# Optimization experiments

Measured on AMD Instinct MI355X. Metric: run time of the kernel, lower is better.

## Reference

```python
import jax, jax.numpy as jnp
import numpy as np

H = 1024

def setup_inputs() -> dict:
    key = jax.random.key(0)
    ks = jax.random.split(key, 7)
    B, S = 64, 2048
    decoder_hidden = jax.random.normal(ks[0], (B, H), dtype=jnp.float32)
    encoder_outputs = jax.random.normal(ks[1], (B, S, H), dtype=jnp.float32)
    sc = 1.0 / np.sqrt(H)
    W1_w = jax.random.normal(ks[2], (H, H), dtype=jnp.float32) * sc
    W1_b = jax.random.normal(ks[3], (H,), dtype=jnp.float32) * sc
    W2_w = jax.random.normal(ks[4], (H, H), dtype=jnp.float32) * sc
    W2_b = jax.random.normal(ks[5], (H,), dtype=jnp.float32) * sc
    v_w = jax.random.normal(ks[6], (H,), dtype=jnp.float32) * sc
    return {"decoder_hidden": decoder_hidden, "encoder_outputs": encoder_outputs,
            "W1_w": W1_w, "W1_b": W1_b, "W2_w": W2_w, "W2_b": W2_b, "v_w": v_w}

def reference(decoder_hidden, encoder_outputs, W1_w, W1_b, W2_w, W2_b, v_w):
    # enc proj: [B,S,H] @ [H,H] ; dec proj: [B,H] @ [H,H], broadcast over S
    enc_proj = jnp.einsum('bsh,hk->bsk', encoder_outputs, W1_w) + W1_b
    dec_proj = decoder_hidden @ W2_w + W2_b  # [B,H]
    e = jnp.tanh(enc_proj + dec_proj[:, None, :])  # [B,S,H]
    scores = jnp.einsum('bsh,h->bs', e, v_w)  # [B,S]
    attn_weights = jax.nn.softmax(scores, axis=1)
    context = jnp.einsum('bs,bsh->bh', attn_weights, encoder_outputs)
    return (context, attn_weights)
```

## Files before the change

### kernel.cpp

```cpp
#include <hip/hip_runtime.h>
#include <hip/hip_bf16.h>
#include <hip/hip_fp16.h>

#define HDIM 1024
#define BATCH 64
#define SEQ 2048
#define MTOT (BATCH*SEQ)
#define BM 128
#define BN 128
#define BK 32

typedef float f32x4 __attribute__((ext_vector_type(4)));
typedef _Float16 half8 __attribute__((ext_vector_type(8)));

static __device__ __forceinline__ void gload_lds16(const void* g, void* l) {
  __builtin_amdgcn_global_load_lds((const __attribute__((address_space(1))) void*)g,
                                   (__attribute__((address_space(3))) void*)l, 16, 0, 0);
}

__global__ void k_w1t(const float* __restrict__ W1, unsigned short* __restrict__ W1T) {
  __shared__ float tile[64][65];
  int h0 = blockIdx.x * 64, k0 = blockIdx.y * 64;
  int t = threadIdx.x;
#pragma unroll
  for (int j = 0; j < 4; ++j) {
    int q = j * 256 + t, r = q >> 4, c = (q & 15) * 4;
    float4 v = *(const float4*)(W1 + (size_t)(h0 + r) * HDIM + k0 + c);
    tile[r][c + 0] = v.x; tile[r][c + 1] = v.y; tile[r][c + 2] = v.z; tile[r][c + 3] = v.w;
  }
  __syncthreads();
#pragma unroll
  for (int j = 0; j < 4; ++j) {
    int q = j * 256 + t, r = q >> 4, c = (q & 15) * 4;
    union { _Float16 h[4]; ushort4 u; } cv;
    cv.h[0] = (_Float16)tile[c + 0][r];
    cv.h[1] = (_Float16)tile[c + 1][r];
    cv.h[2] = (_Float16)tile[c + 2][r];
    cv.h[3] = (_Float16)tile[c + 3][r];
    *(ushort4*)(W1T + (size_t)(k0 + r) * HDIM + h0 + c) = cv.u;
  }
}

__global__ void k_decproj(const float* __restrict__ dh, const float* __restrict__ W2,
                          const float* __restrict__ W2b, float* __restrict__ dp) {
  __shared__ float drow[HDIM];
  int b = blockIdx.x, t = threadIdx.x;
#pragma unroll
  for (int j = 0; j < 4; ++j) drow[j * 256 + t] = dh[(size_t)b * HDIM + j * 256 + t];
  __syncthreads();
  f32x4 acc = {0.f, 0.f, 0.f, 0.f};
#pragma unroll 16
  for (int h = 0; h < HDIM; ++h) {
    float d = drow[h];
    f32x4 w = *(const f32x4*)(W2 + (size_t)h * HDIM + t * 4);
    acc += w * d;
  }
  acc += *(const f32x4*)(W2b + t * 4);
  *(f32x4*)(dp + (size_t)b * HDIM + t * 4) = acc;
}

__global__ __launch_bounds__(256, 2) void k_scores(
    const float* __restrict__ E, const unsigned short* __restrict__ W1T,
    const float* __restrict__ W1b, const float* __restrict__ dp,
    const float* __restrict__ vw, float* __restrict__ spart) {
  __shared__ unsigned short As[BM * BK];
  __shared__ unsigned short Bs[BN * BK];
  __shared__ float biasv[BN], vv[BN];
  __shared__ float scr[BM][2];

  int t = threadIdx.x;
  int bid = blockIdx.x;
  int xcd = bid & 7;
  int q = bid >> 3;
  int mt = (xcd << 7) + (q >> 3);
  int nt = q & 7;
  int m0 = mt * BM, n0 = nt * BN;
  int b = m0 >> 11;

  if (t < BN) {
    int k = n0 + t;
    biasv[t] = W1b[k] + dp[(size_t)b * HDIM + k];
    vv[t] = vw[k];
  }

  int lane = t & 63, wid = t >> 6;
  int wr = wid >> 1, wc = wid & 1;
  int l15 = lane & 15, l4 = lane >> 4;

  f32x4 acc[4][4];
#pragma unroll
  for (int i = 0; i < 4; ++i)
#pragma unroll
    for (int j = 0; j < 4; ++j) acc[i][j] = {0.f, 0.f, 0.f, 0.f};

  const float* Abase = E + (size_t)m0 * HDIM;

  for (int kt = 0; kt < HDIM / BK; ++kt) {
#pragma unroll
    for (int j = 0; j < 4; ++j) {
      int q2 = j * 256 + t;
      int r = q2 >> 3, c = (q2 & 7) * 4;
      float4 v = *(const float4*)(Abase + (size_t)r * HDIM + kt * BK + c);
      union { _Float16 h[4]; unsigned long long u; } cv;
      cv.h[0] = (_Float16)v.x; cv.h[1] = (_Float16)v.y;
      cv.h[2] = (_Float16)v.z; cv.h[3] = (_Float16)v.w;
      *(unsigned long long*)&As[q2 * 4] = cv.u;
    }
#pragma unroll
    for (int j = 0; j < 2; ++j) {
      const unsigned short* g = W1T + (size_t)(n0 + (wid * 2 + j) * 16) * HDIM
                              + (size_t)(lane >> 2) * HDIM
                              + kt * BK + (lane & 3) * 8;
      gload_lds16(g, (char*)Bs + (size_t)(wid * 2 + j) * 1024);
    }
    __syncthreads();

    half8 af[4], bf[4];
#pragma unroll
    for (int mi = 0; mi < 4; ++mi)
      af[mi] = *(const half8*)&As[(wr * 64 + mi * 16 + l15) * BK + l4 * 8];
#pragma unroll
    for (int ni = 0; ni < 4; ++ni)
      bf[ni] = *(const half8*)&Bs[(wc * 64 + ni * 16 + l15) * BK + l4 * 8];
#pragma unroll
    for (int mi = 0; mi < 4; ++mi)
#pragma unroll
      for (int ni = 0; ni < 4; ++ni)
        acc[mi][ni] = __builtin_amdgcn_mfma_f32_16x16x32_f16(af[mi], bf[ni], acc[mi][ni], 0, 0, 0);
    __syncthreads();
  }

  float bias_l[4], v_l[4];
#pragma unroll
  for (int ni = 0; ni < 4; ++ni) {
    bias_l[ni] = biasv[wc * 64 + ni * 16 + l15];
    v_l[ni] = vv[wc * 64 + ni * 16 + l15];
  }
#pragma unroll
  for (int mi = 0; mi < 4; ++mi) {
#pragma unroll
    for (int r = 0; r < 4; ++r) {
      float s = 0.f;
#pragma unroll
      for (int ni = 0; ni < 4; ++ni) {
        float x = acc[mi][ni][r] + bias_l[ni];
        float ex = __expf(2.f * x);
        float th = 1.f - 2.f / (ex + 1.f);
        s += th * v_l[ni];
      }
      s += __shfl_xor(s, 1); s += __shfl_xor(s, 2);
      s += __shfl_xor(s, 4); s += __shfl_xor(s, 8);
      if (l15 == 0) scr[wr * 64 + mi * 16 + l4 * 4 + r][wc] = s;
    }
  }
  __syncthreads();
  if (t < BM) spart[((size_t)m0 + t) * 8 + nt] = scr[t][0] + scr[t][1];
}

__global__ void k_softmax(const float* __restrict__ spart, float* __restrict__ attn) {
  __shared__ float sc[SEQ];
  __shared__ float red[8];
  int b = blockIdx.x, t = threadIdx.x;
  float mx = -1e30f;
#pragma unroll
  for (int j = 0; j < 8; ++j) {
    int s = j * 256 + t;
    const f32x4* p = (const f32x4*)(spart + ((size_t)b * SEQ + s) * 8);
    f32x4 x = p[0], y = p[1];
    float v = (x[0] + x[1]) + (x[2] + x[3]) + (y[0] + y[1]) + (y[2] + y[3]);
    sc[s] = v;
    mx = fmaxf(mx, v);
  }
  for (int m = 1; m < 64; m <<= 1) mx = fmaxf(mx, __shfl_xor(mx, m));
  if ((t & 63) == 0) red[t >> 6] = mx;
  __syncthreads();
  mx = fmaxf(fmaxf(red[0], red[1]), fmaxf(red[2], red[3]));
  float w[8]; float sum = 0.f;
#pragma unroll
  for (int j = 0; j < 8; ++j) {
    float e = __expf(sc[j * 256 + t] - mx);
    w[j] = e; sum += e;
  }
  for (int m = 1; m < 64; m <<= 1) sum += __shfl_xor(sum, m);
  if ((t & 63) == 0) red[4 + (t >> 6)] = sum;
  __syncthreads();
  float inv = 1.f / (red[4] + red[5] + red[6] + red[7]);
#pragma unroll
  for (int j = 0; j < 8; ++j)
    attn[(size_t)b * SEQ + j * 256 + t] = w[j] * inv;
}

__global__ void k_ctx_part(const float* __restrict__ E, const float* __restrict__ attn,
                           float* __restrict__ cpart) {
  int b = blockIdx.x >> 4, ch = blockIdx.x & 15;
  int t = threadIdx.x;
  const float* wrow = attn + (size_t)b * SEQ + ch * 128;
  const float* Eb = E + ((size_t)b * SEQ + ch * 128) * HDIM;
  f32x4 acc = {0.f, 0.f, 0.f, 0.f};
#pragma unroll 4
  for (int s = 0; s < 128; ++s) {
    float w = wrow[s];
    f32x4 e = *(const f32x4*)(Eb + (size_t)s * HDIM + t * 4);
    acc += e * w;
  }
  *(f32x4*)(cpart + (size_t)blockIdx.x * HDIM + t * 4) = acc;
}

__global__ void k_ctx_reduce(const float* __restrict__ cpart, float* __restrict__ ctx) {
  int idx = blockIdx.x * 256 + threadIdx.x;
  int b = idx >> 10, k = idx & 1023;
  float s = 0.f;
#pragma unroll
  for (int c = 0; c < 16; ++c) s += cpart[((size_t)(b * 16 + c)) * HDIM + k];
  ctx[idx] = s;
}

extern "C" void kernel_launch(void* const* d_in, const int* in_sizes, int n_in,
                              void* d_out, int out_size, void* d_ws, size_t ws_size,
                              hipStream_t stream) {
  const float* dh  = (const float*)d_in[0];
  const float* E   = (const float*)d_in[1];
  const float* W1w = (const float*)d_in[2];
  const float* W1b = (const float*)d_in[3];
  const float* W2w = (const float*)d_in[4];
  const float* W2b = (const float*)d_in[5];
  const float* vw  = (const float*)d_in[6];
  float* out  = (float*)d_out;
  float* ctx  = out;
  float* attn = out + BATCH * HDIM;

  char* ws = (char*)d_ws;
  unsigned short* W1T = (unsigned short*)ws;
  float* dp    = (float*)(ws + (2u << 20));
  float* spart = (float*)(ws + (2u << 20) + (256u << 10));
  float* cpart = (float*)(ws + (6u << 20) + (256u << 10));

  k_w1t<<<dim3(16, 16), 256, 0, stream>>>(W1w, W1T);
  k_decproj<<<BATCH, 256, 0, stream>>>(dh, W2w, W2b, dp);
  k_scores<<<(MTOT / BM) * (HDIM / BN), 256, 0, stream>>>(E, W1T, W1b, dp, vw, spart);
  k_softmax<<<BATCH, 256, 0, stream>>>(spart, attn);
  k_ctx_part<<<BATCH * 16, 256, 0, stream>>>(E, attn, cpart);
  k_ctx_reduce<<<256, 256, 0, stream>>>(cpart, ctx);
}
```

Measured before the change: 592.4 us.

## Stream fp32 activations into LDS directly with swizzle, widen K tile, split context more

The score GEMM now loads fp32 encoder tiles straight into LDS with async global-to-LDS copies, using an XOR swizzle to avoid bank conflicts. The fp16 conversion moves to the point where fragments are read from LDS, and BK grows to 64 with two MFMA k-steps per tile. The launch-bounds occupancy hint of 2 is dropped, and the B tile uses a swizzled layout too. The context reduction splits each sequence into 32 chunks when the workspace is large enough, giving more parallelism. The trade-off is doubled LDS per block (fp32 A tile, larger BK), which may lower occupancy, and conversion work repeated per wave in exchange for cutting register staging and VALU work in the load path.

```diff
diff --git a/kernel.cpp b/kernel.cpp
--- a/kernel.cpp
+++ b/kernel.cpp
@@ -8,7 +8,7 @@
 #define MTOT (BATCH*SEQ)
 #define BM 128
 #define BN 128
-#define BK 32
+#define BK 64
 
 typedef float f32x4 __attribute__((ext_vector_type(4)));
 typedef _Float16 half8 __attribute__((ext_vector_type(8)));
@@ -59,11 +59,11 @@
   *(f32x4*)(dp + (size_t)b * HDIM + t * 4) = acc;
 }
 
-__global__ __launch_bounds__(256, 2) void k_scores(
+__global__ __launch_bounds__(256) void k_scores(
     const float* __restrict__ E, const unsigned short* __restrict__ W1T,
     const float* __restrict__ W1b, const float* __restrict__ dp,
     const float* __restrict__ vw, float* __restrict__ spart) {
-  __shared__ unsigned short As[BM * BK];
+  __shared__ float As[BM * BK];
   __shared__ unsigned short Bs[BN * BK];
   __shared__ float biasv[BN], vv[BN];
   __shared__ float scr[BM][2];
@@ -93,40 +93,54 @@
 #pragma unroll
     for (int j = 0; j < 4; ++j) acc[i][j] = {0.f, 0.f, 0.f, 0.f};
 
-  const float* Abase = E + (size_t)m0 * HDIM;
-
   for (int kt = 0; kt < HDIM / BK; ++kt) {
 #pragma unroll
+    for (int j = 0; j < 8; ++j) {
+      int chunk = wid * 8 + j;
+      int row = chunk * 4 + (lane >> 4);
+      int r15 = ((chunk & 3) << 2) + (lane >> 4);
+      int u = (lane & 15) ^ r15;
+      const float* g = E + (size_t)(m0 + row) * HDIM + kt * BK + u * 4;
+      gload_lds16(g, (char*)As + (size_t)chunk * 1024);
+    }
+#pragma unroll
     for (int j = 0; j < 4; ++j) {
-      int q2 = j * 256 + t;
-      int r = q2 >> 3, c = (q2 & 7) * 4;
-      float4 v = *(const float4*)(Abase + (size_t)r * HDIM + kt * BK + c);
-      union { _Float16 h[4]; unsigned long long u; } cv;
-      cv.h[0] = (_Float16)v.x; cv.h[1] = (_Float16)v.y;
-      cv.h[2] = (_Float16)v.z; cv.h[3] = (_Float16)v.w;
-      *(unsigned long long*)&As[q2 * 4] = cv.u;
-    }
-#pragma unroll
-    for (int j = 0; j < 2; ++j) {
-      const unsigned short* g = W1T + (size_t)(n0 + (wid * 2 + j) * 16) * HDIM
-                              + (size_t)(lane >> 2) * HDIM
-                              + kt * BK + (lane & 3) * 8;
-      gload_lds16(g, (char*)Bs + (size_t)(wid * 2 + j) * 1024);
+      int chunk = wid * 4 + j;
+      int row = chunk * 8 + (lane >> 3);
+      int u = (lane & 7) ^ (lane >> 3);
+      const unsigned short* g = W1T + (size_t)(n0 + row) * HDIM + kt * BK + u * 8;
+      gload_lds16(g, (char*)Bs + (size_t)chunk * 1024);
     }
     __syncthreads();
 
-    half8 af[4], bf[4];
-#pragma unroll
-    for (int mi = 0; mi < 4; ++mi)
-      af[mi] = *(const half8*)&As[(wr * 64 + mi * 16 + l15) * BK + l4 * 8];
-#pragma unroll
-    for (int ni = 0; ni < 4; ++ni)
-      bf[ni] = *(const half8*)&Bs[(wc * 64 + ni * 16 + l15) * BK + l4 * 8];
-#pragma unroll
-    for (int mi = 0; mi < 4; ++mi)
-#pragma unroll
-      for (int ni = 0; ni < 4; ++ni)
-        acc[mi][ni] = __builtin_amdgcn_mfma_f32_16x16x32_f16(af[mi], bf[ni], acc[mi][ni], 0, 0, 0);
+#pragma unroll
+    for (int ks = 0; ks < 2; ++ks) {
+      half8 af[4], bf[4];
+#pragma unroll
+      for (int mi = 0; mi < 4; ++mi) {
+        int row = wr * 64 + mi * 16 + l15;
+        int ua = ks * 8 + l4 * 2;
+        f32x4 va = *(const f32x4*)((const char*)As + row * 256 + (((ua    ) ^ l15) << 4));
+        f32x4 vb = *(const f32x4*)((const char*)As + row * 256 + (((ua + 1) ^ l15) << 4));
+        union { _Float16 h[8]; half8 v; } cv;
+        cv.h[0] = (_Float16)va[0]; cv.h[1] = (_Float16)va[1];
+        cv.h[2] = (_Float16)va[2]; cv.h[3] = (_Float16)va[3];
+        cv.h[4] = (_Float16)vb[0]; cv.h[5] = (_Float16)vb[1];
+        cv.h[6] = (_Float16)vb[2]; cv.h[7] = (_Float16)vb[3];
+        af[mi] = cv.v;
+      }
+#pragma unroll
+      for (int ni = 0; ni < 4; ++ni) {
+        int row = wc * 64 + ni * 16 + l15;
+        int u = ks * 4 + l4;
+        bf[ni] = *(const half8*)((const char*)Bs + row * 128 + ((u ^ (l15 & 7)) << 4));
+      }
+#pragma unroll
+      for (int mi = 0; mi < 4; ++mi)
+#pragma unroll
+        for (int ni = 0; ni < 4; ++ni)
+          acc[mi][ni] = __builtin_amdgcn_mfma_f32_16x16x32_f16(af[mi], bf[ni], acc[mi][ni], 0, 0, 0);
+    }
     __syncthreads();
   }
 
@@ -191,14 +205,14 @@
 }
 
 __global__ void k_ctx_part(const float* __restrict__ E, const float* __restrict__ attn,
-                           float* __restrict__ cpart) {
-  int b = blockIdx.x >> 4, ch = blockIdx.x & 15;
+                           float* __restrict__ cpart, int nch, int rpc) {
+  int b = blockIdx.x / nch, ch = blockIdx.x % nch;
   int t = threadIdx.x;
-  const float* wrow = attn + (size_t)b * SEQ + ch * 128;
-  const float* Eb = E + ((size_t)b * SEQ + ch * 128) * HDIM;
+  const float* wrow = attn + (size_t)b * SEQ + (size_t)ch * rpc;
+  const float* Eb = E + ((size_t)b * SEQ + (size_t)ch * rpc) * HDIM;
   f32x4 acc = {0.f, 0.f, 0.f, 0.f};
 #pragma unroll 4
-  for (int s = 0; s < 128; ++s) {
+  for (int s = 0; s < rpc; ++s) {
     float w = wrow[s];
     f32x4 e = *(const f32x4*)(Eb + (size_t)s * HDIM + t * 4);
     acc += e * w;
@@ -206,12 +220,11 @@
   *(f32x4*)(cpart + (size_t)blockIdx.x * HDIM + t * 4) = acc;
 }
 
-__global__ void k_ctx_reduce(const float* __restrict__ cpart, float* __restrict__ ctx) {
+__global__ void k_ctx_reduce(const float* __restrict__ cpart, float* __restrict__ ctx, int nch) {
   int idx = blockIdx.x * 256 + threadIdx.x;
   int b = idx >> 10, k = idx & 1023;
   float s = 0.f;
-#pragma unroll
-  for (int c = 0; c < 16; ++c) s += cpart[((size_t)(b * 16 + c)) * HDIM + k];
+  for (int c = 0; c < nch; ++c) s += cpart[((size_t)(b * nch + c)) * HDIM + k];
   ctx[idx] = s;
 }
 
@@ -235,10 +248,14 @@
   float* spart = (float*)(ws + (2u << 20) + (256u << 10));
   float* cpart = (float*)(ws + (6u << 20) + (256u << 10));
 
+  size_t need32 = (6u << 20) + (256u << 10) + (size_t)BATCH * 32 * HDIM * 4;
+  int nch = (ws_size >= need32) ? 32 : 16;
+  int rpc = SEQ / nch;
+
   k_w1t<<<dim3(16, 16), 256, 0, stream>>>(W1w, W1T);
   k_decproj<<<BATCH, 256, 0, stream>>>(dh, W2w, W2b, dp);
   k_scores<<<(MTOT / BM) * (HDIM / BN), 256, 0, stream>>>(E, W1T, W1b, dp, vw, spart);
   k_softmax<<<BATCH, 256, 0, stream>>>(spart, attn);
-  k_ctx_part<<<BATCH * 16, 256, 0, stream>>>(E, attn, cpart);
-  k_ctx_reduce<<<256, 256, 0, stream>>>(cpart, ctx);
-}
+  k_ctx_part<<<BATCH * nch, 256, 0, stream>>>(E, attn, cpart, nch, rpc);
+  k_ctx_reduce<<<256, 256, 0, stream>>>(cpart, ctx, nch);
+}
```

Measured after the change: 706.9 us. 1.19x slower.
